# Performance work log

Measured on AMD Instinct MI355X. Metric: run time of the kernel, lower is better.

## Reference

```python
import jax, jax.numpy as jnp
import numpy as np

PAD = 0.1
RESO = 128           # plane_resolution
HID = 128            # hidden_dim
CDIM = 128           # c_dim
NBLK = 5             # n_blocks
PLANES = (('xz', (0, 2)), ('xy', (0, 1)), ('yz', (1, 2)))


def normalize_coordinate(p, dims):
    # p: (B,T,3) -> (B,T,2) in [0, 1)
    xy = p[..., list(dims)] / (1.0 + PAD + 1e-3) + 0.5
    return jnp.clip(xy, 0.0, 1.0 - 1e-5)


def coordinate2index(xy, reso):
    g = (xy * reso).astype(jnp.int32)          # (B,T,2)
    return g[..., 0] + reso * g[..., 1]        # (B,T) flat cell index


def scatter_max_gather(vals, idx, n_cells):
    # vals: (B,T,F), idx: (B,T) -> per-cell max gathered back to points (B,T,F)
    B, T, F = vals.shape
    flat_idx = (idx + jnp.arange(B, dtype=idx.dtype)[:, None] * n_cells).reshape(-1)
    fea = jax.ops.segment_max(vals.reshape(B * T, F), flat_idx, num_segments=B * n_cells)
    return fea[flat_idx].reshape(B, T, F)


def scatter_mean_plane(c, idx, n_cells):
    # c: (B,T,C), idx: (B,T) -> (B, n_cells, C); empty cells stay 0
    B, T, C = c.shape
    flat_idx = (idx + jnp.arange(B, dtype=idx.dtype)[:, None] * n_cells).reshape(-1)
    s = jax.ops.segment_sum(c.reshape(B * T, C), flat_idx, num_segments=B * n_cells)
    cnt = jax.ops.segment_sum(jnp.ones((B * T,), c.dtype), flat_idx, num_segments=B * n_cells)
    return (s / jnp.maximum(cnt, 1.0)[:, None]).reshape(B, n_cells, C)


def resnet_block(x, W0, b0, W1, b1, Ws):
    # ResnetBlockFC(2H -> H), size_h = H, shortcut = Linear(no bias)
    net = jax.nn.relu(x) @ W0 + b0
    dx = jax.nn.relu(net) @ W1 + b1
    return x @ Ws + dx


def setup_inputs() -> dict:
    key = jax.random.key(0)
    ks = jax.random.split(key, 10)
    B, T = 2, 32768
    s = 0.05
    return {
        'p': jax.random.uniform(ks[0], (B, T, 3), jnp.float32, -0.5, 0.5),
        'fc_pos_W': s * jax.random.normal(ks[1], (3, 2 * HID), jnp.float32),
        'fc_pos_b': s * jax.random.normal(ks[2], (2 * HID,), jnp.float32),
        'blocks_W0': s * jax.random.normal(ks[3], (NBLK, 2 * HID, HID), jnp.float32),
        'blocks_b0': s * jax.random.normal(ks[4], (NBLK, HID), jnp.float32),
        'blocks_W1': s * jax.random.normal(ks[5], (NBLK, HID, HID), jnp.float32),
        'blocks_b1': s * jax.random.normal(ks[6], (NBLK, HID), jnp.float32),
        'blocks_Ws': s * jax.random.normal(ks[7], (NBLK, 2 * HID, HID), jnp.float32),
        'fc_c_W': s * jax.random.normal(ks[8], (HID, CDIM), jnp.float32),
        'fc_c_b': s * jax.random.normal(ks[9], (CDIM,), jnp.float32),
    }


def reference(p, fc_pos_W, fc_pos_b, blocks_W0, blocks_b0, blocks_W1, blocks_b1,
              blocks_Ws, fc_c_W, fc_c_b):
    B, T, _ = p.shape
    R2 = RESO * RESO
    index = {k: coordinate2index(normalize_coordinate(p, d), RESO) for k, d in PLANES}

    net = p @ fc_pos_W + fc_pos_b                       # (B,T,2H)
    net = resnet_block(net, blocks_W0[0], blocks_b0[0],
                       blocks_W1[0], blocks_b1[0], blocks_Ws[0])  # (B,T,H)
    for i in range(1, NBLK):
        pooled = sum(scatter_max_gather(net, index[k], R2) for k, _ in PLANES)
        net = jnp.concatenate([net, pooled], axis=-1)   # (B,T,2H)
        net = resnet_block(net, blocks_W0[i], blocks_b0[i],
                           blocks_W1[i], blocks_b1[i], blocks_Ws[i])

    c = net @ fc_c_W + fc_c_b                           # (B,T,C)
    planes = []
    for k, _ in PLANES:  # order: xz, xy, yz
        fea = scatter_mean_plane(c, index[k], R2)       # (B,R2,C)
        planes.append(fea.transpose(0, 2, 1).reshape(B, CDIM, RESO, RESO))
    return jnp.stack(planes)                            # (3,B,C,R,R)
```

## Files before the change

### kernel.cpp

```cpp
#include <hip/hip_runtime.h>

#define TT 65536
#define R2 16384

typedef _Float16 f16x8 __attribute__((ext_vector_type(8)));
typedef float    f32x4 __attribute__((ext_vector_type(4)));
typedef unsigned u32x4 __attribute__((ext_vector_type(4)));

#define MFMA16 __builtin_amdgcn_mfma_f32_16x16x32_f16

__device__ __forceinline__ unsigned short f2h(float f){
    _Float16 h = (_Float16)f;
    return __builtin_bit_cast(unsigned short, h);
}
__device__ __forceinline__ float h2f(unsigned short u){
    return (float)__builtin_bit_cast(_Float16, u);
}
__device__ __forceinline__ unsigned relu2(unsigned w){
    unsigned s = w & 0x80008000u;
    unsigned mask = ((s >> 15) * 0x7FFFu) | s;
    return w & ~mask;
}
__device__ __forceinline__ float nrm(float a){
    float v = a / 1.101f + 0.5f;
    v = fmaxf(v, 0.0f);
    v = fminf(v, 0.99999f);
    return v;
}

__global__ __launch_bounds__(256) void k_repack(const float* __restrict__ W0,
        const float* __restrict__ W1, const float* __restrict__ Ws,
        const float* __restrict__ Wc, unsigned short* __restrict__ out){
    int e = blockIdx.x*256 + threadIdx.x;
    const float* src; int r;
    if (e < 409600){
        int i = e / 81920; r = e % 81920;
        if (r < 32768)      { src = W0 + (size_t)i*32768; }
        else if (r < 49152) { src = W1 + (size_t)i*16384; r -= 32768; }
        else                { src = Ws + (size_t)i*32768; r -= 49152; }
    } else { src = Wc; r = e - 409600; }
    int j = r & 7, l = (r >> 3) & 63, t = (r >> 9) & 7, ks = r >> 12;
    int k = ks*32 + (l >> 4)*8 + j;
    int n = t*16 + (l & 15);
    out[e] = f2h(src[k*128 + n]);
}

__global__ __launch_bounds__(256) void k_idxhist(const float* __restrict__ p,
        int* __restrict__ idx, int* __restrict__ cnt){
    int pt = blockIdx.x*256 + threadIdx.x;
    float p0 = p[pt*3+0], p1 = p[pt*3+1], p2 = p[pt*3+2];
    int g0 = (int)(nrm(p0)*128.f);
    int g1 = (int)(nrm(p1)*128.f);
    int g2 = (int)(nrm(p2)*128.f);
    int i0 = g0 + 128*g2, i1 = g0 + 128*g1, i2 = g1 + 128*g2;
    idx[0*TT + pt] = i0;
    idx[1*TT + pt] = i1;
    idx[2*TT + pt] = i2;
    int b14 = (pt >> 15) << 14;
    atomicAdd(&cnt[0*32768 + b14 + i0], 1);
    atomicAdd(&cnt[1*32768 + b14 + i1], 1);
    atomicAdd(&cnt[2*32768 + b14 + i2], 1);
}

__global__ __launch_bounds__(1024) void k_scan(const int* __restrict__ cnt,
        int* __restrict__ cs, int* __restrict__ cp){
    __shared__ int ls[1024];
    int pl = blockIdx.x, tid = threadIdx.x;
    const int* c = cnt + pl*32768;
    int v[32], tot = 0;
    #pragma unroll
    for (int j = 0; j < 32; j++){ v[j] = c[tid*32 + j]; tot += v[j]; }
    int x = tot;
    ls[tid] = x; __syncthreads();
    for (int off = 1; off < 1024; off <<= 1){
        int add = (tid >= off) ? ls[tid - off] : 0;
        __syncthreads();
        x += add; ls[tid] = x;
        __syncthreads();
    }
    int run = x - tot;
    #pragma unroll
    for (int j = 0; j < 32; j++){
        cs[pl*32769 + tid*32 + j] = run;
        cp[pl*32768 + tid*32 + j] = run;
        run += v[j];
    }
    if (tid == 1023) cs[pl*32769 + 32768] = TT;
}

__global__ __launch_bounds__(256) void k_scatter(const int* __restrict__ idx,
        int* __restrict__ cp, int* __restrict__ srt){
    int pt = blockIdx.x*256 + threadIdx.x;
    int b14 = (pt >> 15) << 14;
    #pragma unroll
    for (int pl = 0; pl < 3; pl++){
        int pos = atomicAdd(&cp[pl*32768 + b14 + idx[pl*TT + pt]], 1);
        srt[pl*TT + pos] = pt;
    }
}

__global__ __launch_bounds__(256) void k_pool3(const unsigned short* __restrict__ xb,
        const int* __restrict__ srt, const int* __restrict__ cs,
        unsigned short* __restrict__ mxp){
    int pl = blockIdx.y;
    const int* srtp = srt + (size_t)pl*TT;
    const int* csp  = cs  + (size_t)pl*32769;
    int lane = threadIdx.x & 63;
    int c = blockIdx.x*4 + (threadIdx.x >> 6);
    int s = csp[c], e = csp[c+1];
    if (s == e) return;
    float m0 = -1e30f, m1 = -1e30f;
    int pt = srtp[s];
    for (int i = s; i < e; i++){
        int ptn = (i+1 < e) ? srtp[i+1] : 0;
        unsigned v = ((const unsigned*)(xb + (size_t)pt*256))[lane];
        m0 = fmaxf(m0, h2f((unsigned short)(v & 0xFFFF)));
        m1 = fmaxf(m1, h2f((unsigned short)(v >> 16)));
        pt = ptn;
    }
    unsigned pk = (unsigned)f2h(m0) | ((unsigned)f2h(m1) << 16);
    ((unsigned*)(mxp + ((size_t)pl*32768 + c)*128))[lane] = pk;
}

__global__ __launch_bounds__(256, 2) void k_resnet(unsigned short* __restrict__ xb,
        const unsigned short* __restrict__ wp,
        const float* __restrict__ b0, const float* __restrict__ b1,
        const int* __restrict__ idx, const unsigned short* __restrict__ mxp,
        const float* __restrict__ pin, const float* __restrict__ fW,
        const float* __restrict__ fb,
        const unsigned short* __restrict__ wc, const float* __restrict__ bc){
    __shared__ __align__(16) unsigned short lds[32768];
    unsigned short* lw = lds;
    unsigned short* lt = lds + 16384;
    int tid = threadIdx.x, w = tid >> 6, lane = tid & 63;
    int quad = lane >> 4, l15 = lane & 15;
    int m0 = blockIdx.x*128 + w*32;
    float b0v[8], b1v[8];
    #pragma unroll
    for (int t = 0; t < 8; t++){ b0v[t] = b0[t*16 + l15]; b1v[t] = b1[t*16 + l15]; }

    u32x4 pre[8];
    auto preload = [&](const unsigned short* src){
        const u32x4* g = (const u32x4*)src;
        #pragma unroll
        for (int i = 0; i < 8; i++) pre[i] = g[i*256 + tid];
    };
    auto flush = [&](){
        u32x4* l = (u32x4*)lw;
        #pragma unroll
        for (int i = 0; i < 8; i++) l[i*256 + tid] = pre[i];
    };

    preload(wp);

    u32x4 xf[2][4]; f16x8 pf[2][4];
    if (pin){
        #pragma unroll
        for (int s = 0; s < 2; s++){
            int row = m0 + s*16 + l15;
            float p0 = pin[row*3+0], p1 = pin[row*3+1], p2 = pin[row*3+2];
            #pragma unroll
            for (int ks = 0; ks < 4; ks++){
                int c0 = ks*32 + quad*8;
                unsigned short hx[8], hp[8];
                #pragma unroll
                for (int h = 0; h < 2; h++){
                    f32x4 w0 = *(const f32x4*)(fW + c0 + h*4);
                    f32x4 w1 = *(const f32x4*)(fW + 256 + c0 + h*4);
                    f32x4 w2 = *(const f32x4*)(fW + 512 + c0 + h*4);
                    f32x4 bb = *(const f32x4*)(fb + c0 + h*4);
                    f32x4 v0 = *(const f32x4*)(fW + 128 + c0 + h*4);
                    f32x4 v1 = *(const f32x4*)(fW + 384 + c0 + h*4);
                    f32x4 v2 = *(const f32x4*)(fW + 640 + c0 + h*4);
                    f32x4 bp = *(const f32x4*)(fb + 128 + c0 + h*4);
                    #pragma unroll
                    for (int j = 0; j < 4; j++){
                        hx[h*4+j] = f2h(bb[j] + p0*w0[j] + p1*w1[j] + p2*w2[j]);
                        hp[h*4+j] = f2h(bp[j] + p0*v0[j] + p1*v1[j] + p2*v2[j]);
                    }
                }
                unsigned short* dx = (unsigned short*)&xf[s][ks];
                unsigned short* dp = (unsigned short*)&pf[s][ks];
                #pragma unroll
                for (int j = 0; j < 8; j++){ dx[j] = hx[j]; dp[j] = hp[j]; }
            }
        }
    } else {
        #pragma unroll
        for (int s = 0; s < 2; s++){
            size_t rb = (size_t)(m0 + s*16 + l15)*256;
            #pragma unroll
            for (int ks = 0; ks < 4; ks++)
                xf[s][ks] = *(const u32x4*)(xb + rb + ks*32 + quad*8);
        }
        #pragma unroll
        for (int s = 0; s < 2; s++){
            int row = m0 + s*16 + l15;
            int b14 = (row >> 15) << 14;
            const unsigned short* q0 = mxp + ((size_t)(0*32768 + b14 + idx[row]))*128;
            const unsigned short* q1 = mxp + ((size_t)(1*32768 + b14 + idx[TT + row]))*128;
            const unsigned short* q2 = mxp + ((size_t)(2*32768 + b14 + idx[2*TT + row]))*128;
            #pragma unroll
            for (int ks = 0; ks < 4; ks++){
                int col = ks*32 + quad*8;
                f16x8 a = *(const f16x8*)(q0 + col);
                f16x8 b = *(const f16x8*)(q1 + col);
                f16x8 c = *(const f16x8*)(q2 + col);
                f16x8 r;
                #pragma unroll
                for (int j = 0; j < 8; j++)
                    r[j] = (_Float16)((float)a[j] + (float)b[j] + (float)c[j]);
                pf[s][ks] = r;
            }
        }
    }

    f32x4 acc[2][8];
    #pragma unroll
    for (int s = 0; s < 2; s++)
        #pragma unroll
        for (int t = 0; t < 8; t++){ f32x4 z = {0.f,0.f,0.f,0.f}; acc[s][t] = z; }

    __syncthreads(); flush(); __syncthreads();
    preload(wp + 16384);
    {
        #pragma unroll
        for (int ks = 0; ks < 4; ks++){
            u32x4 u0 = xf[0][ks], u1 = xf[1][ks];
            u0.x = relu2(u0.x); u0.y = relu2(u0.y); u0.z = relu2(u0.z); u0.w = relu2(u0.w);
            u1.x = relu2(u1.x); u1.y = relu2(u1.y); u1.z = relu2(u1.z); u1.w = relu2(u1.w);
            f16x8 a0 = __builtin_bit_cast(f16x8, u0);
            f16x8 a1 = __builtin_bit_cast(f16x8, u1);
            #pragma unroll
            for (int t = 0; t < 8; t++){
                f16x8 b = *(const f16x8*)&lw[((ks*8 + t)*64 + lane)*8];
                acc[0][t] = MFMA16(a0, b, acc[0][t], 0, 0, 0);
                acc[1][t] = MFMA16(a1, b, acc[1][t], 0, 0, 0);
            }
        }
    }

    __syncthreads(); flush(); __syncthreads();
    preload(wp + 32768);
    {
        #pragma unroll
        for (int ks = 0; ks < 4; ks++){
            u32x4 u0 = __builtin_bit_cast(u32x4, pf[0][ks]);
            u32x4 u1 = __builtin_bit_cast(u32x4, pf[1][ks]);
            u0.x = relu2(u0.x); u0.y = relu2(u0.y); u0.z = relu2(u0.z); u0.w = relu2(u0.w);
            u1.x = relu2(u1.x); u1.y = relu2(u1.y); u1.z = relu2(u1.z); u1.w = relu2(u1.w);
            f16x8 a0 = __builtin_bit_cast(f16x8, u0);
            f16x8 a1 = __builtin_bit_cast(f16x8, u1);
            #pragma unroll
            for (int t = 0; t < 8; t++){
                f16x8 b = *(const f16x8*)&lw[((ks*8 + t)*64 + lane)*8];
                acc[0][t] = MFMA16(a0, b, acc[0][t], 0, 0, 0);
                acc[1][t] = MFMA16(a1, b, acc[1][t], 0, 0, 0);
            }
        }
    }

    __syncthreads(); flush(); __syncthreads();
    preload(wp + 49152);
    f32x4 acc2[2][8];
    #pragma unroll
    for (int s = 0; s < 2; s++){
        int strip = w*2 + s;
        #pragma unroll
        for (int t = 0; t < 8; t++){
            int ks2 = t >> 1;
            int l2b = ((t & 1)*2 + ((lane >> 3) & 1))*16 + quad*4;
            #pragma unroll
            for (int r = 0; r < 4; r++){
                float v = acc[s][t][r] + b0v[t];
                v = fmaxf(v, 0.f);
                lt[(((ks2*8 + strip)*64) + l2b + r)*8 + (lane & 7)] = f2h(v);
            }
        }
    }
    #pragma unroll
    for (int s = 0; s < 2; s++)
        #pragma unroll
        for (int t = 0; t < 8; t++){ f32x4 iv = {b1v[t],b1v[t],b1v[t],b1v[t]}; acc2[s][t] = iv; }
    #pragma unroll
    for (int ks = 0; ks < 4; ks++){
        f16x8 a0 = *(const f16x8*)&lt[((ks*8 + w*2 + 0)*64 + lane)*8];
        f16x8 a1 = *(const f16x8*)&lt[((ks*8 + w*2 + 1)*64 + lane)*8];
        #pragma unroll
        for (int t = 0; t < 8; t++){
            f16x8 b = *(const f16x8*)&lw[((ks*8 + t)*64 + lane)*8];
            acc2[0][t] = MFMA16(a0, b, acc2[0][t], 0, 0, 0);
            acc2[1][t] = MFMA16(a1, b, acc2[1][t], 0, 0, 0);
        }
    }

    __syncthreads(); flush(); __syncthreads();
    preload(wp + 65536);
    {
        #pragma unroll
        for (int ks = 0; ks < 4; ks++){
            f16x8 a0 = __builtin_bit_cast(f16x8, xf[0][ks]);
            f16x8 a1 = __builtin_bit_cast(f16x8, xf[1][ks]);
            #pragma unroll
            for (int t = 0; t < 8; t++){
                f16x8 b = *(const f16x8*)&lw[((ks*8 + t)*64 + lane)*8];
                acc2[0][t] = MFMA16(a0, b, acc2[0][t], 0, 0, 0);
                acc2[1][t] = MFMA16(a1, b, acc2[1][t], 0, 0, 0);
            }
        }
    }

    __syncthreads(); flush(); __syncthreads();
    if (wc) preload(wc);
    {
        #pragma unroll
        for (int ks = 0; ks < 4; ks++){
            f16x8 a0 = pf[0][ks];
            f16x8 a1 = pf[1][ks];
            #pragma unroll
            for (int t = 0; t < 8; t++){
                f16x8 b = *(const f16x8*)&lw[((ks*8 + t)*64 + lane)*8];
                acc2[0][t] = MFMA16(a0, b, acc2[0][t], 0, 0, 0);
                acc2[1][t] = MFMA16(a1, b, acc2[1][t], 0, 0, 0);
            }
        }
    }

    if (!wc){
        #pragma unroll
        for (int s = 0; s < 2; s++)
            #pragma unroll
            for (int t = 0; t < 8; t++)
                #pragma unroll
                for (int r = 0; r < 4; r++){
                    int row = m0 + s*16 + quad*4 + r;
                    xb[(size_t)row*256 + t*16 + l15] = f2h(acc2[s][t][r]);
                }
        return;
    }

    __syncthreads(); flush(); __syncthreads();
    #pragma unroll
    for (int s = 0; s < 2; s++){
        int strip = w*2 + s;
        #pragma unroll
        for (int t = 0; t < 8; t++){
            int ks2 = t >> 1;
            int l2b = ((t & 1)*2 + ((lane >> 3) & 1))*16 + quad*4;
            #pragma unroll
            for (int r = 0; r < 4; r++)
                lt[(((ks2*8 + strip)*64) + l2b + r)*8 + (lane & 7)] = f2h(acc2[s][t][r]);
        }
    }
    f32x4 acc3[2][8];
    #pragma unroll
    for (int t = 0; t < 8; t++){
        float bv = bc[t*16 + l15];
        f32x4 iv = {bv, bv, bv, bv};
        acc3[0][t] = iv; acc3[1][t] = iv;
    }
    #pragma unroll
    for (int ks = 0; ks < 4; ks++){
        f16x8 a0 = *(const f16x8*)&lt[((ks*8 + w*2 + 0)*64 + lane)*8];
        f16x8 a1 = *(const f16x8*)&lt[((ks*8 + w*2 + 1)*64 + lane)*8];
        #pragma unroll
        for (int t = 0; t < 8; t++){
            f16x8 b = *(const f16x8*)&lw[((ks*8 + t)*64 + lane)*8];
            acc3[0][t] = MFMA16(a0, b, acc3[0][t], 0, 0, 0);
            acc3[1][t] = MFMA16(a1, b, acc3[1][t], 0, 0, 0);
        }
    }
    #pragma unroll
    for (int s = 0; s < 2; s++)
        #pragma unroll
        for (int t = 0; t < 8; t++)
            #pragma unroll
            for (int r = 0; r < 4; r++){
                int row = m0 + s*16 + quad*4 + r;
                xb[(size_t)row*256 + 128 + t*16 + l15] = f2h(acc3[s][t][r]);
            }
}

__global__ __launch_bounds__(1024) void k_psum3(const unsigned short* __restrict__ xb,
        const int* __restrict__ srt, const int* __restrict__ cs,
        float* __restrict__ out){
    __shared__ float ls[32*129];
    int pl = blockIdx.y;
    const int* srtp = srt + (size_t)pl*TT;
    const int* csp  = cs  + (size_t)pl*32769;
    int w = threadIdx.x >> 6, lane = threadIdx.x & 63;
    int c0 = blockIdx.x * 32;
    #pragma unroll
    for (int cc = w; cc < 32; cc += 16){
        int c = c0 + cc;
        int s = csp[c], e = csp[c+1];
        float s0 = 0.f, s1 = 0.f;
        if (s < e){
            int pt = srtp[s];
            for (int i = s; i < e; i++){
                int ptn = (i+1 < e) ? srtp[i+1] : 0;
                unsigned v = ((const unsigned*)(xb + (size_t)pt*256 + 128))[lane];
                s0 += h2f((unsigned short)(v & 0xFFFF));
                s1 += h2f((unsigned short)(v >> 16));
                pt = ptn;
            }
        }
        float rc = (e > s) ? 1.f/(float)(e - s) : 0.f;
        ls[cc*129 + lane*2]     = s0*rc;
        ls[cc*129 + lane*2 + 1] = s1*rc;
    }
    __syncthreads();
    int pb = pl*2 + (c0 >> 14);
    float* o = out + (size_t)pb*128*R2 + (c0 & 16383);
    #pragma unroll
    for (int j = 0; j < 4; j++){
        int lin = j*1024 + threadIdx.x;
        int f = lin >> 5, cc = lin & 31;
        o[(size_t)f*R2 + cc] = ls[cc*129 + f];
    }
}

extern "C" void kernel_launch(void* const* d_in, const int* in_sizes, int n_in,
                              void* d_out, int out_size, void* d_ws, size_t ws_size,
                              hipStream_t stream) {
    const float* p        = (const float*)d_in[0];
    const float* fc_pos_W = (const float*)d_in[1];
    const float* fc_pos_b = (const float*)d_in[2];
    const float* bW0      = (const float*)d_in[3];
    const float* bb0      = (const float*)d_in[4];
    const float* bW1      = (const float*)d_in[5];
    const float* bb1      = (const float*)d_in[6];
    const float* bWs      = (const float*)d_in[7];
    const float* fc_c_W   = (const float*)d_in[8];
    const float* fc_c_b   = (const float*)d_in[9];
    float* out = (float*)d_out;

    char* ws = (char*)d_ws;
    int*            idx   = (int*)ws;
    unsigned short* xbuf  = (unsigned short*)(ws + 786432);
    int*            srt   = (int*)(ws + 34340864);
    int*            cs    = (int*)(ws + 35127296);
    int*            cp    = (int*)(ws + 35520528);
    unsigned short* wpack = (unsigned short*)(ws + 35913744);
    unsigned short* mxp   = (unsigned short*)(ws + 36765712);

    k_repack<<<1664, 256, 0, stream>>>(bW0, bW1, bWs, fc_c_W, wpack);
    hipMemsetAsync(cp, 0, (size_t)3*32768*4, stream);
    k_idxhist<<<TT/256, 256, 0, stream>>>(p, idx, cp);
    k_scan   <<<3, 1024, 0, stream>>>(cp, cs, cp);
    k_scatter<<<TT/256, 256, 0, stream>>>(idx, cp, srt);

    k_resnet<<<512, 256, 0, stream>>>(xbuf, wpack, bb0, bb1,
            idx, (const unsigned short*)nullptr,
            p, fc_pos_W, fc_pos_b,
            (const unsigned short*)nullptr, (const float*)nullptr);

    for (int i = 1; i < 5; i++){
        k_pool3<<<dim3(8192, 3), 256, 0, stream>>>(xbuf, srt, cs, mxp);
        const unsigned short* wc = (i == 4) ? (wpack + 409600) : (const unsigned short*)nullptr;
        const float* bcp = (i == 4) ? fc_c_b : (const float*)nullptr;
        k_resnet<<<512, 256, 0, stream>>>(xbuf, wpack + (size_t)i*81920,
                bb0 + (size_t)i*128, bb1 + (size_t)i*128,
                idx, mxp,
                (const float*)nullptr, (const float*)nullptr, (const float*)nullptr,
                wc, bcp);
    }

    k_psum3<<<dim3(1024, 3), 1024, 0, stream>>>(xbuf, srt, cs, out);
}
```

Before: 414.3 us.

## Vectorize pooling gathers, warp-shuffle scan, LDS-staged repack with fused memset

The max-pool and mean-pool kernels now have four 16-lane groups each read separate points of a cell using 16-byte vector loads, then combine the partial results with cross-lane shuffles. Each wave now handles several cells in a loop, and the launch grids are resized to match. The weight repack stages tiles in LDS to make both reads and writes coalesced, and it also zeroes the histogram counts, which removes the separate memset call. The scan replaces its LDS Hillis-Steele loop with wave shuffles. The goal is fewer scalar gathers, fewer launches and fewer barriers, at the cost of more per-lane registers and shuffle reductions.

```diff
diff --git a/kernel.cpp b/kernel.cpp
--- a/kernel.cpp
+++ b/kernel.cpp
@@ -30,19 +30,43 @@
 
 __global__ __launch_bounds__(256) void k_repack(const float* __restrict__ W0,
         const float* __restrict__ W1, const float* __restrict__ Ws,
-        const float* __restrict__ Wc, unsigned short* __restrict__ out){
-    int e = blockIdx.x*256 + threadIdx.x;
-    const float* src; int r;
-    if (e < 409600){
-        int i = e / 81920; r = e % 81920;
-        if (r < 32768)      { src = W0 + (size_t)i*32768; }
-        else if (r < 49152) { src = W1 + (size_t)i*16384; r -= 32768; }
-        else                { src = Ws + (size_t)i*32768; r -= 49152; }
-    } else { src = Wc; r = e - 409600; }
-    int j = r & 7, l = (r >> 3) & 63, t = (r >> 9) & 7, ks = r >> 12;
-    int k = ks*32 + (l >> 4)*8 + j;
-    int n = t*16 + (l & 15);
-    out[e] = f2h(src[k*128 + n]);
+        const float* __restrict__ Wc, unsigned short* __restrict__ out,
+        int* __restrict__ cnt){
+    __shared__ unsigned short lh[4096];
+    int b = blockIdx.x, tid = threadIdx.x;
+
+    int gid = b*256 + tid;
+    if (gid < 24576){ u32x4 z = {0,0,0,0}; ((u32x4*)cnt)[gid] = z; }
+
+    const float* src; int obase;
+    if (b < 100){
+        int i = b/20, rr = b%20;
+        if (rr < 8){       src = W0 + (size_t)i*32768 + rr*4096;      obase = i*81920 + rr*4096; }
+        else if (rr < 12){ int ks=rr-8;  src = W1 + (size_t)i*16384 + ks*4096; obase = i*81920 + 32768 + ks*4096; }
+        else {             int ks=rr-12; src = Ws + (size_t)i*32768 + ks*4096; obase = i*81920 + 49152 + ks*4096; }
+    } else { int ks = b-100; src = Wc + ks*4096; obase = 409600 + ks*4096; }
+
+    #pragma unroll
+    for (int m = 0; m < 16; m++){
+        int gi = m*256 + tid;
+        lh[gi] = f2h(src[gi]);
+    }
+    __syncthreads();
+
+    #pragma unroll
+    for (int g2 = 0; g2 < 2; g2++){
+        int base = tid*16 + g2*8;
+        int l = (base >> 3) & 63, t = (base >> 9) & 7;
+        int n = t*16 + (l & 15), kb = (l >> 4)*8;
+        unsigned short h[8];
+        #pragma unroll
+        for (int j = 0; j < 8; j++) h[j] = lh[(kb + j)*128 + n];
+        u32x4 pk;
+        #pragma unroll
+        for (int q = 0; q < 4; q++)
+            pk[q] = (unsigned)h[2*q] | ((unsigned)h[2*q+1] << 16);
+        *(u32x4*)(&out[obase + base]) = pk;
+    }
 }
 
 __global__ __launch_bounds__(256) void k_idxhist(const float* __restrict__ p,
@@ -64,21 +88,25 @@
 
 __global__ __launch_bounds__(1024) void k_scan(const int* __restrict__ cnt,
         int* __restrict__ cs, int* __restrict__ cp){
-    __shared__ int ls[1024];
+    __shared__ int wsum[16];
     int pl = blockIdx.x, tid = threadIdx.x;
+    int lane = tid & 63, wid = tid >> 6;
     const int* c = cnt + pl*32768;
     int v[32], tot = 0;
     #pragma unroll
     for (int j = 0; j < 32; j++){ v[j] = c[tid*32 + j]; tot += v[j]; }
     int x = tot;
-    ls[tid] = x; __syncthreads();
-    for (int off = 1; off < 1024; off <<= 1){
-        int add = (tid >= off) ? ls[tid - off] : 0;
-        __syncthreads();
-        x += add; ls[tid] = x;
-        __syncthreads();
-    }
-    int run = x - tot;
+    #pragma unroll
+    for (int off = 1; off < 64; off <<= 1){
+        int y = __shfl_up(x, off, 64);
+        if (lane >= off) x += y;
+    }
+    if (lane == 63) wsum[wid] = x;
+    __syncthreads();
+    int woff = 0;
+    #pragma unroll
+    for (int j = 0; j < 16; j++) woff += (j < wid) ? wsum[j] : 0;
+    int run = woff + x - tot;
     #pragma unroll
     for (int j = 0; j < 32; j++){
         cs[pl*32769 + tid*32 + j] = run;
@@ -105,21 +133,38 @@
     int pl = blockIdx.y;
     const int* srtp = srt + (size_t)pl*TT;
     const int* csp  = cs  + (size_t)pl*32769;
-    int lane = threadIdx.x & 63;
-    int c = blockIdx.x*4 + (threadIdx.x >> 6);
-    int s = csp[c], e = csp[c+1];
-    if (s == e) return;
-    float m0 = -1e30f, m1 = -1e30f;
-    int pt = srtp[s];
-    for (int i = s; i < e; i++){
-        int ptn = (i+1 < e) ? srtp[i+1] : 0;
-        unsigned v = ((const unsigned*)(xb + (size_t)pt*256))[lane];
-        m0 = fmaxf(m0, h2f((unsigned short)(v & 0xFFFF)));
-        m1 = fmaxf(m1, h2f((unsigned short)(v >> 16)));
-        pt = ptn;
-    }
-    unsigned pk = (unsigned)f2h(m0) | ((unsigned)f2h(m1) << 16);
-    ((unsigned*)(mxp + ((size_t)pl*32768 + c)*128))[lane] = pk;
+    int lane = threadIdx.x & 63, w = threadIdx.x >> 6;
+    int g = lane >> 4, l16 = lane & 15;
+    int cbase = (blockIdx.x*4 + w)*4;
+    for (int c = cbase; c < cbase + 4; c++){
+        int s = csp[c], e = csp[c+1];
+        if (s == e) continue;
+        float fm[8];
+        #pragma unroll
+        for (int j = 0; j < 8; j++) fm[j] = -1e30f;
+        for (int i = s + g; i < e; i += 4){
+            int pt = srtp[i];
+            u32x4 v = *(const u32x4*)(xb + (size_t)pt*256 + l16*8);
+            #pragma unroll
+            for (int q = 0; q < 4; q++){
+                unsigned u = v[q];
+                fm[2*q]   = fmaxf(fm[2*q],   h2f((unsigned short)(u & 0xFFFF)));
+                fm[2*q+1] = fmaxf(fm[2*q+1], h2f((unsigned short)(u >> 16)));
+            }
+        }
+        #pragma unroll
+        for (int j = 0; j < 8; j++){
+            fm[j] = fmaxf(fm[j], __shfl_xor(fm[j], 16, 64));
+            fm[j] = fmaxf(fm[j], __shfl_xor(fm[j], 32, 64));
+        }
+        if (g == 0){
+            u32x4 pk;
+            #pragma unroll
+            for (int q = 0; q < 4; q++)
+                pk[q] = (unsigned)f2h(fm[2*q]) | ((unsigned)f2h(fm[2*q+1]) << 16);
+            ((u32x4*)(mxp + ((size_t)pl*32768 + c)*128))[l16] = pk;
+        }
+    }
 }
 
 __global__ __launch_bounds__(256, 2) void k_resnet(unsigned short* __restrict__ xb,
@@ -381,40 +426,50 @@
             }
 }
 
-__global__ __launch_bounds__(1024) void k_psum3(const unsigned short* __restrict__ xb,
+__global__ __launch_bounds__(256) void k_psum3(const unsigned short* __restrict__ xb,
         const int* __restrict__ srt, const int* __restrict__ cs,
         float* __restrict__ out){
     __shared__ float ls[32*129];
     int pl = blockIdx.y;
     const int* srtp = srt + (size_t)pl*TT;
     const int* csp  = cs  + (size_t)pl*32769;
-    int w = threadIdx.x >> 6, lane = threadIdx.x & 63;
+    int tid = threadIdx.x;
+    int lane = tid & 63, w = tid >> 6;
+    int g = lane >> 4, l16 = lane & 15;
     int c0 = blockIdx.x * 32;
-    #pragma unroll
-    for (int cc = w; cc < 32; cc += 16){
+    for (int cc = w*8; cc < w*8 + 8; cc++){
         int c = c0 + cc;
         int s = csp[c], e = csp[c+1];
-        float s0 = 0.f, s1 = 0.f;
-        if (s < e){
-            int pt = srtp[s];
-            for (int i = s; i < e; i++){
-                int ptn = (i+1 < e) ? srtp[i+1] : 0;
-                unsigned v = ((const unsigned*)(xb + (size_t)pt*256 + 128))[lane];
-                s0 += h2f((unsigned short)(v & 0xFFFF));
-                s1 += h2f((unsigned short)(v >> 16));
-                pt = ptn;
-            }
+        float fs[8];
+        #pragma unroll
+        for (int j = 0; j < 8; j++) fs[j] = 0.f;
+        for (int i = s + g; i < e; i += 4){
+            int pt = srtp[i];
+            u32x4 v = *(const u32x4*)(xb + (size_t)pt*256 + 128 + l16*8);
+            #pragma unroll
+            for (int q = 0; q < 4; q++){
+                unsigned u = v[q];
+                fs[2*q]   += h2f((unsigned short)(u & 0xFFFF));
+                fs[2*q+1] += h2f((unsigned short)(u >> 16));
+            }
+        }
+        #pragma unroll
+        for (int j = 0; j < 8; j++){
+            fs[j] += __shfl_xor(fs[j], 16, 64);
+            fs[j] += __shfl_xor(fs[j], 32, 64);
         }
         float rc = (e > s) ? 1.f/(float)(e - s) : 0.f;
-        ls[cc*129 + lane*2]     = s0*rc;
-        ls[cc*129 + lane*2 + 1] = s1*rc;
+        if (g == 0){
+            #pragma unroll
+            for (int j = 0; j < 8; j++) ls[cc*129 + l16*8 + j] = fs[j]*rc;
+        }
     }
     __syncthreads();
     int pb = pl*2 + (c0 >> 14);
     float* o = out + (size_t)pb*128*R2 + (c0 & 16383);
     #pragma unroll
-    for (int j = 0; j < 4; j++){
-        int lin = j*1024 + threadIdx.x;
+    for (int k = 0; k < 16; k++){
+        int lin = k*256 + tid;
         int f = lin >> 5, cc = lin & 31;
         o[(size_t)f*R2 + cc] = ls[cc*129 + f];
     }
@@ -444,8 +499,7 @@
     unsigned short* wpack = (unsigned short*)(ws + 35913744);
     unsigned short* mxp   = (unsigned short*)(ws + 36765712);
 
-    k_repack<<<1664, 256, 0, stream>>>(bW0, bW1, bWs, fc_c_W, wpack);
-    hipMemsetAsync(cp, 0, (size_t)3*32768*4, stream);
+    k_repack <<<104, 256, 0, stream>>>(bW0, bW1, bWs, fc_c_W, wpack, cp);
     k_idxhist<<<TT/256, 256, 0, stream>>>(p, idx, cp);
     k_scan   <<<3, 1024, 0, stream>>>(cp, cs, cp);
     k_scatter<<<TT/256, 256, 0, stream>>>(idx, cp, srt);
@@ -456,7 +510,7 @@
             (const unsigned short*)nullptr, (const float*)nullptr);
 
     for (int i = 1; i < 5; i++){
-        k_pool3<<<dim3(8192, 3), 256, 0, stream>>>(xbuf, srt, cs, mxp);
+        k_pool3<<<dim3(2048, 3), 256, 0, stream>>>(xbuf, srt, cs, mxp);
         const unsigned short* wc = (i == 4) ? (wpack + 409600) : (const unsigned short*)nullptr;
         const float* bcp = (i == 4) ? fc_c_b : (const float*)nullptr;
         k_resnet<<<512, 256, 0, stream>>>(xbuf, wpack + (size_t)i*81920,
@@ -466,5 +520,5 @@
                 wc, bcp);
     }
 
-    k_psum3<<<dim3(1024, 3), 1024, 0, stream>>>(xbuf, srt, cs, out);
-}
+    k_psum3<<<dim3(1024, 3), 256, 0, stream>>>(xbuf, srt, cs, out);
+}
```

Result: faster. 376.6 us (-9.1%).
